# Kernel tuning notes

Measured on AMD Instinct MI355X. Metric: run time of the kernel, lower is better.

Reference implementation:

```python
import jax, jax.numpy as jnp
import numpy as np


def setup_inputs() -> dict:
    key = jax.random.key(0)
    k1, k2 = jax.random.split(key)
    n, c, h, w = 32, 256, 64, 64
    x = jax.random.normal(k1, (n, c, h, w), dtype=jnp.float32)
    tau = jax.random.uniform(k2, (), dtype=jnp.float32)  # blend factor in (0,1)
    return {"x": x, "tau": tau, "topk_keep_num": 409}


def reference(x, tau, topk_keep_num):
    # x: [n, c, h, w]; keep top-k |x| entries over the flattened h*w axis per (n, c).
    n, c, h, w = x.shape
    hw = h * w
    if topk_keep_num == hw:
        return x
    xr = x.reshape(n, c, hw)
    # top-k indices by absolute value along last axis
    _, idx = jax.lax.top_k(jnp.abs(xr), topk_keep_num)  # idx: [n, c, k]
    # scatter ones at selected positions (torch.zeros_like(...).scatter_(2, idx, 1))
    bi = jnp.arange(n)[:, None, None]
    ci = jnp.arange(c)[None, :, None]
    mask = jnp.zeros_like(xr).at[bi, ci, idx].set(1.0)
    sparse_x = (mask * xr).reshape(n, c, h, w)
    # blend: sparse_x * tau + x * (1 - tau)  (tau == 1.0 reduces to sparse_x)
    return sparse_x * tau + x * (1.0 - tau)
```

## Files before the change

kernel.cpp:

```cpp
#include <hip/hip_runtime.h>
#include <hip/hip_bf16.h>

#define TPB 256
#define HW 4096
#define NB 4096

typedef unsigned int u32;
typedef unsigned long long u64;

__global__ void __launch_bounds__(TPB)
topk_blend_kernel(const float* __restrict__ x, const float* __restrict__ taup,
                  const int* __restrict__ kp, float* __restrict__ out)
{
    __shared__ u32 hist[NB];
    __shared__ u32 waveTot[4];
    __shared__ u32 sh_b, sh_k1, sh_cnt, sh_pstar;

    const int tid  = threadIdx.x;
    const int lane = tid & 63;
    const int wv   = tid >> 6;
    const int row  = blockIdx.x;

    const float4* xr  = reinterpret_cast<const float4*>(x + (size_t)row * HW);
    float4*       orw = reinterpret_cast<float4*>(out + (size_t)row * HW);

    uint4* h4 = reinterpret_cast<uint4*>(hist);
    const uint4 z4 = make_uint4(0u, 0u, 0u, 0u);
#pragma unroll
    for (int j = 0; j < NB / 4 / TPB; ++j) h4[tid + j * TPB] = z4;
    if (tid == 0) sh_cnt = 0;

    u32 r[16];
#pragma unroll
    for (int j = 0; j < 4; ++j) {
        float4 v = xr[tid + j * TPB];
        r[4 * j + 0] = __float_as_uint(v.x);
        r[4 * j + 1] = __float_as_uint(v.y);
        r[4 * j + 2] = __float_as_uint(v.z);
        r[4 * j + 3] = __float_as_uint(v.w);
    }
    const u32  K   = (u32)(*kp);
    const float tau = *taup;
    __syncthreads();

    if (K >= HW) {
#pragma unroll
        for (int j = 0; j < 4; ++j) {
            float4 o;
            o.x = __uint_as_float(r[4 * j + 0]);
            o.y = __uint_as_float(r[4 * j + 1]);
            o.z = __uint_as_float(r[4 * j + 2]);
            o.w = __uint_as_float(r[4 * j + 3]);
            orw[tid + j * TPB] = o;
        }
        return;
    }

#pragma unroll
    for (int e = 0; e < 16; ++e)
        atomicAdd(&hist[(r[e] & 0x7fffffffu) >> 19], 1u);
    __syncthreads();

    u32 hh[16];
    {
        uint4 a0 = h4[tid * 4 + 0], a1 = h4[tid * 4 + 1];
        uint4 a2 = h4[tid * 4 + 2], a3 = h4[tid * 4 + 3];
        hh[0]=a0.x; hh[1]=a0.y; hh[2]=a0.z;  hh[3]=a0.w;
        hh[4]=a1.x; hh[5]=a1.y; hh[6]=a1.z;  hh[7]=a1.w;
        hh[8]=a2.x; hh[9]=a2.y; hh[10]=a2.z; hh[11]=a2.w;
        hh[12]=a3.x;hh[13]=a3.y;hh[14]=a3.z; hh[15]=a3.w;
    }
    u32 s = 0;
#pragma unroll
    for (int j = 0; j < 16; ++j) s += hh[j];

    u32 suf = s;
#pragma unroll
    for (int d = 1; d < 64; d <<= 1) {
        u32 t = __shfl_down(suf, d, 64);
        if (lane + d < 64) suf += t;
    }
    if (lane == 0) waveTot[wv] = suf;
    __syncthreads();
    u32 above = suf - s;
#pragma unroll
    for (int w2 = 0; w2 < 4; ++w2)
        if (w2 > wv) above += waveTot[w2];

    if (above < K && above + s >= K) {
        u32 c = above;
        int fb = -1; u32 kk = 0;
#pragma unroll
        for (int bi = 15; bi >= 0; --bi) {
            u32 hb = hh[bi];
            if (fb < 0) {
                if (c + hb >= K) { fb = bi; kk = K - c; }
                else c += hb;
            }
        }
        sh_b  = (u32)(tid * 16 + fb);
        sh_k1 = kk;
    }
    __syncthreads();

    const u32 bstar = sh_b;
    const u32 k1    = sh_k1;

    u32* cand = hist;
#pragma unroll
    for (int e = 0; e < 16; ++e) {
        u32 key = r[e] & 0x7fffffffu;
        bool inb = ((key >> 19) == bstar);
        u64 m = __ballot(inb);
        if (m) {
            int leader = (int)(__ffsll((long long)m) - 1);
            u32 base = 0;
            if (lane == leader) base = atomicAdd(&sh_cnt, (u32)__popcll(m));
            base = __shfl(base, leader, 64);
            if (inb) {
                int j = e >> 2, l = e & 3;
                u32 idx  = (u32)((((j * TPB + tid) << 2) | l));
                u32 pack = ((key & 0x7ffffu) << 12) | (4095u - idx);
                cand[base + (u32)__popcll(m & ((1ull << lane) - 1ull))] = pack;
            }
        }
    }
    __syncthreads();

    const u32 ceq = sh_cnt;
    for (u32 i = tid; i < ceq; i += TPB) {
        u32 p  = cand[i];
        u32 rk = 0;
        for (u32 j2 = 0; j2 < ceq; ++j2)
            rk += (cand[j2] > p) ? 1u : 0u;
        if (rk == k1 - 1u) sh_pstar = p;
    }
    __syncthreads();
    const u32 pstar = sh_pstar;

    const float om = 1.0f - tau;
#pragma unroll
    for (int j = 0; j < 4; ++j) {
        float4 o;
        float* po = reinterpret_cast<float*>(&o);
#pragma unroll
        for (int l = 0; l < 4; ++l) {
            int e = 4 * j + l;
            u32 rb   = r[e];
            u32 key  = rb & 0x7fffffffu;
            u32 bin  = key >> 19;
            u32 idx  = (u32)((((j * TPB + tid) << 2) | l));
            u32 pack = ((key & 0x7ffffu) << 12) | (4095u - idx);
            bool keep = (bin > bstar) || (bin == bstar && pack >= pstar);
            float xv = __uint_as_float(rb);
            po[l] = keep ? (xv * tau + xv * om) : (xv * om);
        }
        orw[tid + j * TPB] = o;
    }
}

extern "C" void kernel_launch(void* const* d_in, const int* in_sizes, int n_in,
                              void* d_out, int out_size, void* d_ws, size_t ws_size,
                              hipStream_t stream)
{
    (void)n_in; (void)out_size; (void)d_ws; (void)ws_size;
    const float* x   = (const float*)d_in[0];
    const float* tau = (const float*)d_in[1];
    const int*   kp  = (const int*)d_in[2];
    float*       out = (float*)d_out;
    const int nrows  = in_sizes[0] / HW;
    topk_blend_kernel<<<nrows, TPB, 0, stream>>>(x, tau, kp, out);
}
```

Baseline: 232.3 us.

## Process four rows per block with register double-buffered prefetch of next row

Each block now handles four rows and loads the next row into a second register set while the current row runs its histogram and select phases, to hide global load latency behind LDS work. It also XOR-swizzles histogram bins to reduce LDS bank conflicts, replaces the ballot-based candidate compaction with per-lane atomics, uses nontemporal stores for the output, and sets a minimum-occupancy launch bound. The extra registers may reduce occupancy, and the grid is a quarter the size. Row count must be divisible by four.

```diff
diff --git a/kernel.cpp b/kernel.cpp
--- a/kernel.cpp
+++ b/kernel.cpp
@@ -4,11 +4,13 @@
 #define TPB 256
 #define HW 4096
 #define NB 4096
+#define RPB 4
 
 typedef unsigned int u32;
 typedef unsigned long long u64;
+typedef float floatx4 __attribute__((ext_vector_type(4)));
 
-__global__ void __launch_bounds__(TPB)
+__global__ void __launch_bounds__(TPB, 6)
 topk_blend_kernel(const float* __restrict__ x, const float* __restrict__ taup,
                   const int* __restrict__ kp, float* __restrict__ out)
 {
@@ -19,144 +21,145 @@
     const int tid  = threadIdx.x;
     const int lane = tid & 63;
     const int wv   = tid >> 6;
-    const int row  = blockIdx.x;
+    const int row0 = blockIdx.x * RPB;
 
-    const float4* xr  = reinterpret_cast<const float4*>(x + (size_t)row * HW);
-    float4*       orw = reinterpret_cast<float4*>(out + (size_t)row * HW);
-
-    uint4* h4 = reinterpret_cast<uint4*>(hist);
-    const uint4 z4 = make_uint4(0u, 0u, 0u, 0u);
-#pragma unroll
-    for (int j = 0; j < NB / 4 / TPB; ++j) h4[tid + j * TPB] = z4;
-    if (tid == 0) sh_cnt = 0;
-
-    u32 r[16];
-#pragma unroll
-    for (int j = 0; j < 4; ++j) {
-        float4 v = xr[tid + j * TPB];
-        r[4 * j + 0] = __float_as_uint(v.x);
-        r[4 * j + 1] = __float_as_uint(v.y);
-        r[4 * j + 2] = __float_as_uint(v.z);
-        r[4 * j + 3] = __float_as_uint(v.w);
-    }
     const u32  K   = (u32)(*kp);
     const float tau = *taup;
-    __syncthreads();
+    const float om  = 1.0f - tau;
+    const u32  xm  = (u32)(tid & 31);
 
     if (K >= HW) {
+        for (int i = 0; i < RPB; ++i) {
+            const float4* xr = reinterpret_cast<const float4*>(x + (size_t)(row0 + i) * HW);
+            float4*       ow = reinterpret_cast<float4*>(out + (size_t)(row0 + i) * HW);
 #pragma unroll
-        for (int j = 0; j < 4; ++j) {
-            float4 o;
-            o.x = __uint_as_float(r[4 * j + 0]);
-            o.y = __uint_as_float(r[4 * j + 1]);
-            o.z = __uint_as_float(r[4 * j + 2]);
-            o.w = __uint_as_float(r[4 * j + 3]);
-            orw[tid + j * TPB] = o;
+            for (int j = 0; j < 4; ++j) ow[tid + j * TPB] = xr[tid + j * TPB];
         }
         return;
     }
 
+    u32 rA[16], rB[16];
+    {
+        const float4* xr = reinterpret_cast<const float4*>(x + (size_t)row0 * HW);
 #pragma unroll
-    for (int e = 0; e < 16; ++e)
-        atomicAdd(&hist[(r[e] & 0x7fffffffu) >> 19], 1u);
-    __syncthreads();
+        for (int j = 0; j < 4; ++j) {
+            float4 v = xr[tid + j * TPB];
+            rA[4*j+0] = __float_as_uint(v.x); rA[4*j+1] = __float_as_uint(v.y);
+            rA[4*j+2] = __float_as_uint(v.z); rA[4*j+3] = __float_as_uint(v.w);
+        }
+    }
 
-    u32 hh[16];
-    {
-        uint4 a0 = h4[tid * 4 + 0], a1 = h4[tid * 4 + 1];
-        uint4 a2 = h4[tid * 4 + 2], a3 = h4[tid * 4 + 3];
-        hh[0]=a0.x; hh[1]=a0.y; hh[2]=a0.z;  hh[3]=a0.w;
-        hh[4]=a1.x; hh[5]=a1.y; hh[6]=a1.z;  hh[7]=a1.w;
-        hh[8]=a2.x; hh[9]=a2.y; hh[10]=a2.z; hh[11]=a2.w;
-        hh[12]=a3.x;hh[13]=a3.y;hh[14]=a3.z; hh[15]=a3.w;
-    }
-    u32 s = 0;
+    auto process = [&](u32 (&r)[16], u32 (&rn)[16], int row, int nrow) {
+        if (nrow >= 0) {
+            const float4* xr = reinterpret_cast<const float4*>(x + (size_t)nrow * HW);
 #pragma unroll
-    for (int j = 0; j < 16; ++j) s += hh[j];
-
-    u32 suf = s;
-#pragma unroll
-    for (int d = 1; d < 64; d <<= 1) {
-        u32 t = __shfl_down(suf, d, 64);
-        if (lane + d < 64) suf += t;
-    }
-    if (lane == 0) waveTot[wv] = suf;
-    __syncthreads();
-    u32 above = suf - s;
-#pragma unroll
-    for (int w2 = 0; w2 < 4; ++w2)
-        if (w2 > wv) above += waveTot[w2];
-
-    if (above < K && above + s >= K) {
-        u32 c = above;
-        int fb = -1; u32 kk = 0;
-#pragma unroll
-        for (int bi = 15; bi >= 0; --bi) {
-            u32 hb = hh[bi];
-            if (fb < 0) {
-                if (c + hb >= K) { fb = bi; kk = K - c; }
-                else c += hb;
+            for (int j = 0; j < 4; ++j) {
+                float4 v = xr[tid + j * TPB];
+                rn[4*j+0] = __float_as_uint(v.x); rn[4*j+1] = __float_as_uint(v.y);
+                rn[4*j+2] = __float_as_uint(v.z); rn[4*j+3] = __float_as_uint(v.w);
             }
         }
-        sh_b  = (u32)(tid * 16 + fb);
-        sh_k1 = kk;
-    }
-    __syncthreads();
 
-    const u32 bstar = sh_b;
-    const u32 k1    = sh_k1;
+        uint4* h4 = reinterpret_cast<uint4*>(hist);
+        const uint4 z4 = make_uint4(0u, 0u, 0u, 0u);
+#pragma unroll
+        for (int j = 0; j < NB / 4 / TPB; ++j) h4[tid + j * TPB] = z4;
+        if (tid == 0) sh_cnt = 0;
+        __syncthreads();
 
-    u32* cand = hist;
 #pragma unroll
-    for (int e = 0; e < 16; ++e) {
-        u32 key = r[e] & 0x7fffffffu;
-        bool inb = ((key >> 19) == bstar);
-        u64 m = __ballot(inb);
-        if (m) {
-            int leader = (int)(__ffsll((long long)m) - 1);
-            u32 base = 0;
-            if (lane == leader) base = atomicAdd(&sh_cnt, (u32)__popcll(m));
-            base = __shfl(base, leader, 64);
-            if (inb) {
-                int j = e >> 2, l = e & 3;
+        for (int e = 0; e < 16; ++e) {
+            u32 bin = (r[e] & 0x7fffffffu) >> 19;
+            atomicAdd(&hist[bin ^ ((bin >> 4) & 31u)], 1u);
+        }
+        __syncthreads();
+
+        u32 hh[16];
+        u32 s = 0;
+#pragma unroll
+        for (int j = 0; j < 16; ++j) {
+            hh[j] = hist[(u32)(tid * 16 + j) ^ xm];
+            s += hh[j];
+        }
+        u32 suf = s;
+#pragma unroll
+        for (int d = 1; d < 64; d <<= 1) {
+            u32 t = __shfl_down(suf, d, 64);
+            if (lane + d < 64) suf += t;
+        }
+        if (lane == 0) waveTot[wv] = suf;
+        __syncthreads();
+        u32 above = suf - s;
+#pragma unroll
+        for (int w2 = 0; w2 < 4; ++w2)
+            if (w2 > wv) above += waveTot[w2];
+
+        if (above < K && above + s >= K) {
+            u32 c = above;
+            int fb = -1; u32 kk = 0;
+#pragma unroll
+            for (int bi = 15; bi >= 0; --bi) {
+                u32 hb = hh[bi];
+                if (fb < 0) {
+                    if (c + hb >= K) { fb = bi; kk = K - c; }
+                    else c += hb;
+                }
+            }
+            sh_b  = (u32)(tid * 16 + fb);
+            sh_k1 = kk;
+        }
+        __syncthreads();
+
+        const u32 bstar = sh_b;
+        const u32 k1    = sh_k1;
+
+        u32* cand = hist;
+#pragma unroll
+        for (int e = 0; e < 16; ++e) {
+            u32 key = r[e] & 0x7fffffffu;
+            if ((key >> 19) == bstar) {
+                u32 pos = atomicAdd(&sh_cnt, 1u);
+                u32 idx = (u32)((((e >> 2) * TPB + tid) << 2) | (e & 3));
+                cand[pos] = ((key & 0x7ffffu) << 12) | (4095u - idx);
+            }
+        }
+        __syncthreads();
+
+        const u32 ceq = sh_cnt;
+        for (u32 i = tid; i < ceq; i += TPB) {
+            u32 p  = cand[i];
+            u32 rk = 0;
+            for (u32 j2 = 0; j2 < ceq; ++j2)
+                rk += (cand[j2] > p) ? 1u : 0u;
+            if (rk == k1 - 1u) sh_pstar = p;
+        }
+        __syncthreads();
+        const u32 pstar = sh_pstar;
+
+        floatx4* ow = reinterpret_cast<floatx4*>(out + (size_t)row * HW);
+#pragma unroll
+        for (int j = 0; j < 4; ++j) {
+            floatx4 o;
+#pragma unroll
+            for (int l = 0; l < 4; ++l) {
+                int e = 4 * j + l;
+                u32 rb   = r[e];
+                u32 key  = rb & 0x7fffffffu;
+                u32 bin  = key >> 19;
                 u32 idx  = (u32)((((j * TPB + tid) << 2) | l));
                 u32 pack = ((key & 0x7ffffu) << 12) | (4095u - idx);
-                cand[base + (u32)__popcll(m & ((1ull << lane) - 1ull))] = pack;
+                bool keep = (bin > bstar) || (bin == bstar && pack >= pstar);
+                float xv = __uint_as_float(rb);
+                o[l] = keep ? (xv * tau + xv * om) : (xv * om);
             }
+            __builtin_nontemporal_store(o, &ow[tid + j * TPB]);
         }
-    }
-    __syncthreads();
+    };
 
-    const u32 ceq = sh_cnt;
-    for (u32 i = tid; i < ceq; i += TPB) {
-        u32 p  = cand[i];
-        u32 rk = 0;
-        for (u32 j2 = 0; j2 < ceq; ++j2)
-            rk += (cand[j2] > p) ? 1u : 0u;
-        if (rk == k1 - 1u) sh_pstar = p;
-    }
-    __syncthreads();
-    const u32 pstar = sh_pstar;
-
-    const float om = 1.0f - tau;
-#pragma unroll
-    for (int j = 0; j < 4; ++j) {
-        float4 o;
-        float* po = reinterpret_cast<float*>(&o);
-#pragma unroll
-        for (int l = 0; l < 4; ++l) {
-            int e = 4 * j + l;
-            u32 rb   = r[e];
-            u32 key  = rb & 0x7fffffffu;
-            u32 bin  = key >> 19;
-            u32 idx  = (u32)((((j * TPB + tid) << 2) | l));
-            u32 pack = ((key & 0x7ffffu) << 12) | (4095u - idx);
-            bool keep = (bin > bstar) || (bin == bstar && pack >= pstar);
-            float xv = __uint_as_float(rb);
-            po[l] = keep ? (xv * tau + xv * om) : (xv * om);
-        }
-        orw[tid + j * TPB] = o;
-    }
+    process(rA, rB, row0 + 0, row0 + 1);
+    process(rB, rA, row0 + 1, row0 + 2);
+    process(rA, rB, row0 + 2, row0 + 3);
+    process(rB, rA, row0 + 3, -1);
 }
 
 extern "C" void kernel_launch(void* const* d_in, const int* in_sizes, int n_in,
@@ -169,5 +172,5 @@
     const int*   kp  = (const int*)d_in[2];
     float*       out = (float*)d_out;
     const int nrows  = in_sizes[0] / HW;
-    topk_blend_kernel<<<nrows, TPB, 0, stream>>>(x, tau, kp, out);
+    topk_blend_kernel<<<nrows / RPB, TPB, 0, stream>>>(x, tau, kp, out);
 }
```

Result: slower. 282.3 us (+21.5%).
